# Kernel optimization log

Measured on AMD Instinct MI355X. Metric: run time of the kernel, lower is better.

## Reference

```python
import jax, jax.numpy as jnp
import numpy as np

B, T, D, H, KH, HD, F, L, V = 2, 2048, 1024, 16, 4, 64, 4096, 4, 32000
G = H // KH  # num_key_value_groups
EPS = 1e-6
SCALE = HD ** -0.5


def setup_inputs() -> dict:
    key = jax.random.key(0)
    ks = jax.random.split(key, 8)
    std = 0.02
    return {
        "input_ids": jax.random.randint(ks[0], (B, T), 0, V, dtype=jnp.int32),
        "embed_w": jax.random.normal(ks[1], (V, D), jnp.float32) * std,
        "pos_w": jax.random.normal(ks[2], (T, D), jnp.float32) * std,
        "ln1_w": jnp.ones((L, D), jnp.float32),
        "ln2_w": jnp.ones((L, D), jnp.float32),
        "wq": jax.random.normal(ks[3], (L, D, H * HD), jnp.float32) * std,
        "wkv": jax.random.normal(ks[4], (L, D, 2 * KH * HD), jnp.float32) * std,
        "wo": jax.random.normal(ks[5], (L, H * HD, D), jnp.float32) * std,
        "w1": jax.random.normal(ks[6], (L, D, F), jnp.float32) * std,
        "w2": jax.random.normal(ks[7], (L, F, D), jnp.float32) * std,
        "norm_w": jnp.ones((D,), jnp.float32),
    }


def _rmsnorm(x, w):
    return x * jax.lax.rsqrt(jnp.mean(x * x, axis=-1, keepdims=True) + EPS) * w


def reference(input_ids, embed_w, pos_w, ln1_w, ln2_w, wq, wkv, wo, w1, w2, norm_w):
    causal = jnp.tril(jnp.ones((T, T), dtype=bool))  # True = keep
    x = embed_w[input_ids] + pos_w[:T]  # [B,T,D]
    for l in range(L):
        h = _rmsnorm(x, ln1_w[l])
        q = (h @ wq[l]).reshape(B, T, H, HD)
        kv = h @ wkv[l]
        k, v = jnp.split(kv, 2, axis=-1)
        k = jnp.repeat(k.reshape(B, T, KH, HD), G, axis=2)  # GQA repeat_interleave
        v = jnp.repeat(v.reshape(B, T, KH, HD), G, axis=2)
        scores = jnp.einsum("bqhd,bkhd->bhqk", q, k) * SCALE
        scores = jnp.where(causal, scores, -jnp.inf)
        p = jax.nn.softmax(scores, axis=-1)
        o = jnp.einsum("bhqk,bkhd->bqhd", p, v).reshape(B, T, H * HD)
        x = x + o @ wo[l]
        h = _rmsnorm(x, ln2_w[l])
        x = x + jax.nn.gelu(h @ w1[l], approximate=False) @ w2[l]
    x = _rmsnorm(x, norm_w)
    logits = x @ embed_w.T  # tied lm_head
    return logits
```

## Files before the change

kernel.cpp:

```cpp
#include <hip/hip_runtime.h>
#include <hip/hip_bf16.h>

#define DI __device__ __forceinline__

typedef unsigned short u16;
typedef unsigned int u32;
typedef __attribute__((ext_vector_type(8))) short bf16x8;
typedef __attribute__((ext_vector_type(4))) short bf16x4;
typedef __attribute__((ext_vector_type(4))) float f32x4;

#define B_   2
#define T_   2048
#define D_   1024
#define H_   16
#define KH_  4
#define HD_  64
#define F_   4096
#define L_   4
#define V_   32000
#define M_   (B_ * T_)
#define QKVN (H_*HD_ + 2*KH_*HD_)

DI u16 f2bf(float f) {
  __hip_bfloat16 h = __float2bfloat16(f);
  return *reinterpret_cast<u16*>(&h);
}

DI float bf2f(u16 b) {
  __hip_bfloat16 h = *reinterpret_cast<__hip_bfloat16*>(&b);
  return __bfloat162float(h);
}

DI void gl_lds16(const void* g, void* l) {
  __builtin_amdgcn_global_load_lds(
      (const __attribute__((address_space(1))) u32*)g,
      (__attribute__((address_space(3))) u32*)l, 16, 0, 0);
}

#define BARRIER() do { asm volatile("" ::: "memory"); __builtin_amdgcn_s_barrier(); asm volatile("" ::: "memory"); } while (0)
#define LGK0()    asm volatile("s_waitcnt lgkmcnt(0)" ::: "memory")
#define VMC(n)    asm volatile("s_waitcnt vmcnt(" #n ")" ::: "memory")
#define PRIO(p)   __builtin_amdgcn_s_setprio(p)

__global__ __launch_bounds__(256) void embed_kernel(const int* __restrict__ ids,
                                                    const float* __restrict__ ew,
                                                    const float* __restrict__ pw,
                                                    float* __restrict__ x) {
  const int row = blockIdx.x;
  const int t = row & (T_ - 1);
  const int id = ids[row];
  float4 e = reinterpret_cast<const float4*>(ew + (size_t)id * D_)[threadIdx.x];
  float4 p = reinterpret_cast<const float4*>(pw + (size_t)t * D_)[threadIdx.x];
  e.x += p.x; e.y += p.y; e.z += p.z; e.w += p.w;
  reinterpret_cast<float4*>(x + (size_t)row * D_)[threadIdx.x] = e;
}

__global__ __launch_bounds__(256) void conv_kernel(const float* __restrict__ W,
                                                   u16* __restrict__ Wb) {
  const size_t i = (size_t)blockIdx.x * 256 + threadIdx.x;
  float4 v = reinterpret_cast<const float4*>(W)[i];
  ushort4 ov;
  ov.x = f2bf(v.x); ov.y = f2bf(v.y); ov.z = f2bf(v.z); ov.w = f2bf(v.w);
  reinterpret_cast<ushort4*>(Wb)[i] = ov;
}

__global__ __launch_bounds__(256) void convt_fused(const float* __restrict__ wq,
                                                   const float* __restrict__ wkv,
                                                   const float* __restrict__ wo,
                                                   const float* __restrict__ w1,
                                                   const float* __restrict__ w2,
                                                   u16* __restrict__ wtq,
                                                   u16* __restrict__ wto,
                                                   u16* __restrict__ wt1,
                                                   u16* __restrict__ wt2) {
  const int t = blockIdx.x;
  const float* W; u16* Wt; int K, N, local;
  if (t < 1024)      { W = wq;  Wt = wtq;               K = 1024; N = 1024; local = t; }
  else if (t < 1536) { W = wkv; Wt = wtq + 1024*1024;   K = 1024; N = 512;  local = t - 1024; }
  else if (t < 2560) { W = wo;  Wt = wto;               K = 1024; N = 1024; local = t - 1536; }
  else if (t < 6656) { W = w1;  Wt = wt1;               K = 1024; N = 4096; local = t - 2560; }
  else               { W = w2;  Wt = wt2;               K = 4096; N = 1024; local = t - 6656; }
  const int nk = K >> 5;
  const int k0 = (local % nk) * 32, n0 = (local / nk) * 32;
  __shared__ float tb[32][33];
  const int tx = threadIdx.x & 31, ty = threadIdx.x >> 5;
  #pragma unroll
  for (int i = 0; i < 4; i++)
    tb[ty + i*8][tx] = W[(size_t)(k0 + ty + i*8) * N + n0 + tx];
  __syncthreads();
  #pragma unroll
  for (int i = 0; i < 4; i++)
    Wt[(size_t)(n0 + ty + i*8) * K + k0 + tx] = f2bf(tb[tx][ty + i*8]);
}

__global__ __launch_bounds__(256) void rmsnorm_kernel(const float* __restrict__ x,
                                                      const float* __restrict__ w,
                                                      u16* __restrict__ out) {
  const int row = blockIdx.x;
  const int tid = threadIdx.x;
  float4 v = reinterpret_cast<const float4*>(x + (size_t)row * D_)[tid];
  float ss = v.x*v.x + v.y*v.y + v.z*v.z + v.w*v.w;
  #pragma unroll
  for (int off = 32; off > 0; off >>= 1) ss += __shfl_down(ss, off, 64);
  __shared__ float red[4];
  if ((tid & 63) == 0) red[tid >> 6] = ss;
  __syncthreads();
  const float tot = red[0] + red[1] + red[2] + red[3];
  const float rstd = rsqrtf(tot * (1.0f / D_) + 1e-6f);
  float4 wv = reinterpret_cast<const float4*>(w)[tid];
  ushort4 ov;
  ov.x = f2bf(v.x * rstd * wv.x);
  ov.y = f2bf(v.y * rstd * wv.y);
  ov.z = f2bf(v.z * rstd * wv.z);
  ov.w = f2bf(v.w * rstd * wv.w);
  reinterpret_cast<ushort4*>(out + (size_t)row * D_)[tid] = ov;
}

template <int EPI>
__global__ __launch_bounds__(256) void gemm_bt(const u16* __restrict__ A,
                                               const u16* __restrict__ Bt,
                                               const float* __restrict__ res,
                                               u16* __restrict__ Cb,
                                               float* __restrict__ Cf,
                                               int M, int N, int K) {
  __shared__ u16 As[128 * 64];
  __shared__ u16 Bs[128 * 64];
  const int tid = threadIdx.x;
  const int n0 = blockIdx.x * 128;
  const int m0 = blockIdx.y * 128;
  const int lane = tid & 63, wave = tid >> 6;
  const int wm = wave >> 1, wn = wave & 1;
  const int l15 = lane & 15, l4 = lane >> 4;
  const int srow = tid >> 3, scol = (tid & 7) * 8;
  const u16* ag = A + (size_t)(m0 + srow) * K + scol;
  const u16* bg = Bt + (size_t)(n0 + srow) * K + scol;
  u16* asd = &As[srow * 64 + scol];
  u16* bsd = &Bs[srow * 64 + scol];
  f32x4 acc[4][4] = {};
  const int nk = K >> 6;
  for (int kt = 0; kt < nk; kt++) {
    const int k0 = kt * 64;
    __syncthreads();
    #pragma unroll
    for (int i = 0; i < 4; i++) gl_lds16(ag + (size_t)i*32*K + k0, asd + i*32*64);
    #pragma unroll
    for (int i = 0; i < 4; i++) gl_lds16(bg + (size_t)i*32*K + k0, bsd + i*32*64);
    __syncthreads();
    #pragma unroll
    for (int s = 0; s < 2; s++) {
      bf16x8 af[4], bfv[4];
      #pragma unroll
      for (int i = 0; i < 4; i++)
        af[i] = *reinterpret_cast<const bf16x8*>(&As[(wm*64 + i*16 + l15)*64 + s*32 + l4*8]);
      #pragma unroll
      for (int j = 0; j < 4; j++)
        bfv[j] = *reinterpret_cast<const bf16x8*>(&Bs[(wn*64 + j*16 + l15)*64 + s*32 + l4*8]);
      #pragma unroll
      for (int i = 0; i < 4; i++)
        #pragma unroll
        for (int j = 0; j < 4; j++)
          acc[i][j] = __builtin_amdgcn_mfma_f32_16x16x32_bf16(bfv[j], af[i], acc[i][j], 0, 0, 0);
    }
  }
  #pragma unroll
  for (int i = 0; i < 4; i++) {
    const int row = m0 + wm*64 + i*16 + l15;
    #pragma unroll
    for (int j = 0; j < 4; j++) {
      const int colb = n0 + wn*64 + j*16 + l4*4;
      const size_t idx = (size_t)row * N + colb;
      const f32x4 v = acc[i][j];
      if (EPI == 0) {
        ushort4 ov;
        ov.x = f2bf(v[0]); ov.y = f2bf(v[1]); ov.z = f2bf(v[2]); ov.w = f2bf(v[3]);
        *reinterpret_cast<ushort4*>(&Cb[idx]) = ov;
      } else {
        const float4 rv = *reinterpret_cast<const float4*>(&res[idx]);
        float4 ov;
        ov.x = v[0] + rv.x; ov.y = v[1] + rv.y; ov.z = v[2] + rv.z; ov.w = v[3] + rv.w;
        *reinterpret_cast<float4*>(&Cf[idx]) = ov;
      }
    }
  }
}

template <int EPI>
__global__ __launch_bounds__(512, 2) void gemm256(const u16* __restrict__ A,
                                                  const u16* __restrict__ Bt,
                                                  u16* __restrict__ Cb,
                                                  float* __restrict__ Cf,
                                                  int M, int N, int K) {
  __shared__ char lds[131072];
  char* const AsB = lds;
  char* const BsB = lds + 65536;
  const int tid = threadIdx.x;
  const int lane = tid & 63, wave = tid >> 6;
  const int wm = wave >> 2, wn = wave & 3;
  const int l15 = lane & 15, l4 = lane >> 4;

  const int nm = M >> 8;
  const int nwg = nm * (N >> 8);
  const int cpx = nwg >> 3;
  const int bid = blockIdx.x;
  const int wg = (bid & 7) * cpx + (bid >> 3);
  const int m0 = (wg % nm) << 8;
  const int n0 = (wg / nm) << 8;

  const u16* const Atile = A + (size_t)m0 * K;
  const u16* const Btile = Bt + (size_t)n0 * K;

  int soff[2][2], pd[2][2];
  #pragma unroll
  for (int h = 0; h < 2; ++h)
    #pragma unroll
    for (int jj = 0; jj < 2; ++jj) {
      const int row = h*128 + jj*64 + (tid >> 3);
      const int sl  = (tid & 7) ^ (row & 7);
      soff[h][jj] = row * K + sl * 8;
      pd[h][jj]   = h*16384 + jj*8192 + tid*16;
    }
  const int swz = (l15 & 7) << 4;
  const int rb0 = l15*128 + ((l4*16)      ^ swz);
  const int rb1 = l15*128 + ((64 + l4*16) ^ swz);

  #define STA(S,H,T) do { const u16* g_ = Atile + (T)*64; char* d_ = AsB + (S)*32768; \
      gl_lds16(g_ + soff[H][0], d_ + pd[H][0]); gl_lds16(g_ + soff[H][1], d_ + pd[H][1]); } while (0)
  #define STB(S,H,T) do { const u16* g_ = Btile + (T)*64; char* d_ = BsB + (S)*32768; \
      gl_lds16(g_ + soff[H][0], d_ + pd[H][0]); gl_lds16(g_ + soff[H][1], d_ + pd[H][1]); } while (0)
  #define RDA(S,GI,RB) (*reinterpret_cast<const bf16x8*>(AsB + (S)*32768 + (GI)*2048 + (RB)))
  #define RDB(S,GJ,RB) (*reinterpret_cast<const bf16x8*>(BsB + (S)*32768 + (GJ)*2048 + (RB)))

  f32x4 acc[8][4] = {};
  bf16x8 Ar[4][2], Br[4][2];

  #define RDA03(S) { _Pragma("unroll") for (int i=0;i<4;++i){ Ar[i][0]=RDA(S,i*2+wm,rb0); Ar[i][1]=RDA(S,i*2+wm,rb1);} }
  #define RDA47(S) { _Pragma("unroll") for (int i=0;i<4;++i){ Ar[i][0]=RDA(S,(i+4)*2+wm,rb0); Ar[i][1]=RDA(S,(i+4)*2+wm,rb1);} }
  #define RDB01(S) { _Pragma("unroll") for (int j=0;j<2;++j){ Br[j][0]=RDB(S,j*4+wn,rb0); Br[j][1]=RDB(S,j*4+wn,rb1);} }
  #define RDB23(S) { _Pragma("unroll") for (int j=2;j<4;++j){ Br[j][0]=RDB(S,j*4+wn,rb0); Br[j][1]=RDB(S,j*4+wn,rb1);} }
  #define MFQ(IO,JL) { _Pragma("unroll") for (int i=0;i<4;++i) _Pragma("unroll") for (int jj=0;jj<2;++jj) { \
      acc[(IO)+i][(JL)+jj] = __builtin_amdgcn_mfma_f32_16x16x32_bf16(Br[(JL)+jj][0], Ar[i][0], acc[(IO)+i][(JL)+jj],0,0,0); \
      acc[(IO)+i][(JL)+jj] = __builtin_amdgcn_mfma_f32_16x16x32_bf16(Br[(JL)+jj][1], Ar[i][1], acc[(IO)+i][(JL)+jj],0,0,0); } }

  STA(0,0,0); STA(0,1,0); STB(0,0,0); STB(0,1,0);
  VMC(4);
  STA(1,0,1); STB(1,0,1); STB(1,1,1);
  VMC(6);
  BARRIER();

  const int niter = K >> 7;
  for (int it = 0; it < niter; ++it) {
    const int t0 = it*2, t1 = t0 + 1;
    const bool pf = (it + 1 < niter);
    RDA03(0); RDB01(0); STA(1,1,t1);
    BARRIER(); LGK0(); PRIO(1); MFQ(0,0); PRIO(0); BARRIER();
    RDB23(0); if (pf) STA(0,0,t0+2);
    BARRIER(); LGK0(); PRIO(1); MFQ(0,2); PRIO(0); BARRIER();
    RDA47(0); if (pf) STB(0,0,t0+2);
    BARRIER(); LGK0(); PRIO(1); MFQ(4,0); PRIO(0); BARRIER();
    if (pf) { STB(0,1,t0+2); VMC(6); } else { VMC(0); }
    BARRIER(); PRIO(1); MFQ(4,2); PRIO(0); BARRIER();
    RDA03(1); RDB01(1); if (pf) STA(0,1,t0+2);
    BARRIER(); LGK0(); PRIO(1); MFQ(0,0); PRIO(0); BARRIER();
    RDB23(1); if (pf) STA(1,0,t1+2);
    BARRIER(); LGK0(); PRIO(1); MFQ(0,2); PRIO(0); BARRIER();
    RDA47(1); if (pf) STB(1,0,t1+2);
    BARRIER(); LGK0(); PRIO(1); MFQ(4,0); PRIO(0); BARRIER();
    if (pf) { STB(1,1,t1+2); VMC(6); }
    BARRIER(); PRIO(1); MFQ(4,2); PRIO(0); BARRIER();
  }

  #pragma unroll
  for (int i = 0; i < 8; ++i) {
    const int row = m0 + (i*2 + wm)*16 + l15;
    #pragma unroll
    for (int j = 0; j < 4; ++j) {
      const int colb = n0 + (j*4 + wn)*16 + l4*4;
      const f32x4 v = acc[i][j];
      if (EPI == 0) {
        *reinterpret_cast<f32x4*>(&Cf[(size_t)row * N + colb]) = v;
      } else {
        ushort4 ov;
        #pragma unroll
        for (int rr = 0; rr < 4; ++rr) {
          const float g = 0.5f * v[rr] * (1.0f + erff(v[rr] * 0.70710678118f));
          ((u16*)&ov)[rr] = f2bf(g);
        }
        *reinterpret_cast<ushort4*>(&Cb[(size_t)row * N + colb]) = ov;
      }
    }
  }
  #undef STA
  #undef STB
  #undef RDA
  #undef RDB
  #undef RDA03
  #undef RDA47
  #undef RDB01
  #undef RDB23
  #undef MFQ
}

__global__ __launch_bounds__(512) void attn_kernel(const u16* __restrict__ qkv,
                                                   u16* __restrict__ o) {
  const int qtA = blockIdx.x;
  const int qtB = 15 - qtA;
  const int h  = blockIdx.y;
  const int b  = blockIdx.z;
  const int kh = h / (H_ / KH_);
  __shared__ u16 Ks[2][64 * 64];
  __shared__ u16 Vt[64 * 66];
  __shared__ u16 Pl[16][16 * 68];
  const int tid = threadIdx.x, lane = tid & 63, wave = tid >> 6;
  const int l15 = lane & 15, l4 = lane >> 4;
  const size_t Mrow = (size_t)b * T_;

  bf16x8 qfA[2], qfB[2];
  {
    const u16* qpA = qkv + (Mrow + qtA*128 + wave*16 + l15) * QKVN + h*HD_ + l4*8;
    const u16* qpB = qkv + (Mrow + qtB*128 + wave*16 + l15) * QKVN + h*HD_ + l4*8;
    qfA[0] = *reinterpret_cast<const bf16x8*>(qpA);
    qfA[1] = *reinterpret_cast<const bf16x8*>(qpA + 32);
    qfB[0] = *reinterpret_cast<const bf16x8*>(qpB);
    qfB[1] = *reinterpret_cast<const bf16x8*>(qpB + 32);
    #pragma unroll
    for (int s = 0; s < 2; s++)
      #pragma unroll
      for (int j = 0; j < 8; j++) {
        qfA[s][j] = (short)f2bf(bf2f((u16)qfA[s][j]) * 0.18033688f);
        qfB[s][j] = (short)f2bf(bf2f((u16)qfB[s][j]) * 0.18033688f);
      }
  }
  float mA = -1e30f, lA = 0.0f, mB = -1e30f, lB = 0.0f;
  f32x4 oaccA[4] = {}, oaccB[4] = {};

  const int srow = tid >> 3, scol = (tid & 7) * 8;
  const int vp = (tid >> 4) * 2;
  const int vd = (tid & 15) * 4;
  const u16* const kbase = qkv + Mrow * QKVN + D_ + kh*HD_;
  const u16* const vbase = kbase + KH_*HD_;

  {
    gl_lds16(kbase + (size_t)srow * QKVN + scol, &Ks[0][srow*64 + scol]);
    const u16* vg = vbase + (size_t)vp * QKVN + vd;
    bf16x4 v0 = *reinterpret_cast<const bf16x4*>(vg);
    bf16x4 v1 = *reinterpret_cast<const bf16x4*>(vg + QKVN);
    #pragma unroll
    for (int j = 0; j < 4; j++) {
      const u32 pk = (u32)(u16)v0[j] | ((u32)(u16)v1[j] << 16);
      *reinterpret_cast<u32*>(&Vt[(vd + j)*66 + vp]) = pk;
    }
  }
  __syncthreads();

  const int nktA = 2*qtA + 2;
  const int nktB = 2*qtB + 2;
  for (int kt = 0; kt < nktB; kt++) {
    const int cur = kt & 1;
    const bool pf = kt + 1 < nktB;
    bf16x4 v0n, v1n;
    if (pf) {
      gl_lds16(kbase + (size_t)((kt+1)*64 + srow) * QKVN + scol,
               &Ks[1-cur][srow*64 + scol]);
      const u16* vg = vbase + (size_t)((kt+1)*64 + vp) * QKVN + vd;
      v0n = *reinterpret_cast<const bf16x4*>(vg);
      v1n = *reinterpret_cast<const bf16x4*>(vg + QKVN);
    }

    {
      f32x4 sa[4] = {};
      #pragma unroll
      for (int s = 0; s < 2; s++)
        #pragma unroll
        for (int n = 0; n < 4; n++) {
          bf16x8 kf = *reinterpret_cast<const bf16x8*>(&Ks[cur][(n*16 + l15)*64 + s*32 + l4*8]);
          sa[n] = __builtin_amdgcn_mfma_f32_16x16x32_bf16(kf, qfB[s], sa[n], 0, 0, 0);
        }
      if (kt >= 2*qtB) {
        const int qloc = wave*16 + l15;
        const int kb = kt*64 - qtB*128 + l4*4;
        #pragma unroll
        for (int n = 0; n < 4; n++)
          #pragma unroll
          for (int r = 0; r < 4; r++)
            if (kb + n*16 + r > qloc) sa[n][r] = -1e30f;
      }
      float mx;
      {
        f32x4 m4;
        #pragma unroll
        for (int r = 0; r < 4; r++)
          m4[r] = fmaxf(fmaxf(sa[0][r], sa[1][r]), fmaxf(sa[2][r], sa[3][r]));
        mx = fmaxf(fmaxf(m4[0], m4[1]), fmaxf(m4[2], m4[3]));
        mx = fmaxf(mx, __shfl_xor(mx, 16, 64));
        mx = fmaxf(mx, __shfl_xor(mx, 32, 64));
      }
      if (__any((int)(mx - mB > 8.0f))) {
        const float nm = fmaxf(mB, mx);
        const float alpha = exp2f(mB - nm);
        mB = nm; lB *= alpha;
        #pragma unroll
        for (int r = 0; r < 4; r++) {
          const float a_r = __shfl(alpha, l4*4 + r, 64);
          #pragma unroll
          for (int n = 0; n < 4; n++) oaccB[n][r] *= a_r;
        }
      }
      float rs = 0.0f;
      u16* pw = &Pl[8 + wave][0];
      #pragma unroll
      for (int n = 0; n < 4; n++) {
        ushort4 pv;
        #pragma unroll
        for (int r = 0; r < 4; r++) {
          const float p = exp2f(sa[n][r] - mB);
          rs += p;
          ((u16*)&pv)[r] = f2bf(p);
        }
        *reinterpret_cast<ushort4*>(&pw[l15*68 + n*16 + l4*4]) = pv;
      }
      rs += __shfl_xor(rs, 16, 64);
      rs += __shfl_xor(rs, 32, 64);
      lB += rs;
      asm volatile("s_waitcnt lgkmcnt(0)" ::: "memory");
      #pragma unroll
      for (int s = 0; s < 2; s++) {
        bf16x8 pa = *reinterpret_cast<const bf16x8*>(&pw[l15*68 + s*32 + l4*8]);
        #pragma unroll
        for (int n = 0; n < 4; n++) {
          bf16x8 vb = *reinterpret_cast<const bf16x8*>(&Vt[(n*16 + l15)*66 + s*32 + l4*8]);
          oaccB[n] = __builtin_amdgcn_mfma_f32_16x16x32_bf16(pa, vb, oaccB[n], 0, 0, 0);
        }
      }
    }

    if (kt < nktA) {
      f32x4 sa[4] = {};
      #pragma unroll
      for (int s = 0; s < 2; s++)
        #pragma unroll
        for (int n = 0; n < 4; n++) {
          bf16x8 kf = *reinterpret_cast<const bf16x8*>(&Ks[cur][(n*16 + l15)*64 + s*32 + l4*8]);
          sa[n] = __builtin_amdgcn_mfma_f32_16x16x32_bf16(kf, qfA[s], sa[n], 0, 0, 0);
        }
      if (kt >= 2*qtA) {
        const int qloc = wave*16 + l15;
        const int kb = kt*64 - qtA*128 + l4*4;
        #pragma unroll
        for (int n = 0; n < 4; n++)
          #pragma unroll
          for (int r = 0; r < 4; r++)
            if (kb + n*16 + r > qloc) sa[n][r] = -1e30f;
      }
      float mx;
      {
        f32x4 m4;
        #pragma unroll
        for (int r = 0; r < 4; r++)
          m4[r] = fmaxf(fmaxf(sa[0][r], sa[1][r]), fmaxf(sa[2][r], sa[3][r]));
        mx = fmaxf(fmaxf(m4[0], m4[1]), fmaxf(m4[2], m4[3]));
        mx = fmaxf(mx, __shfl_xor(mx, 16, 64));
        mx = fmaxf(mx, __shfl_xor(mx, 32, 64));
      }
      if (__any((int)(mx - mA > 8.0f))) {
        const float nm = fmaxf(mA, mx);
        const float alpha = exp2f(mA - nm);
        mA = nm; lA *= alpha;
        #pragma unroll
        for (int r = 0; r < 4; r++) {
          const float a_r = __shfl(alpha, l4*4 + r, 64);
          #pragma unroll
          for (int n = 0; n < 4; n++) oaccA[n][r] *= a_r;
        }
      }
      float rs = 0.0f;
      u16* pw = &Pl[wave][0];
      #pragma unroll
      for (int n = 0; n < 4; n++) {
        ushort4 pv;
        #pragma unroll
        for (int r = 0; r < 4; r++) {
          const float p = exp2f(sa[n][r] - mA);
          rs += p;
          ((u16*)&pv)[r] = f2bf(p);
        }
        *reinterpret_cast<ushort4*>(&pw[l15*68 + n*16 + l4*4]) = pv;
      }
      rs += __shfl_xor(rs, 16, 64);
      rs += __shfl_xor(rs, 32, 64);
      lA += rs;
      asm volatile("s_waitcnt lgkmcnt(0)" ::: "memory");
      #pragma unroll
      for (int s = 0; s < 2; s++) {
        bf16x8 pa = *reinterpret_cast<const bf16x8*>(&pw[l15*68 + s*32 + l4*8]);
        #pragma unroll
        for (int n = 0; n < 4; n++) {
          bf16x8 vb = *reinterpret_cast<const bf16x8*>(&Vt[(n*16 + l15)*66 + s*32 + l4*8]);
          oaccA[n] = __builtin_amdgcn_mfma_f32_16x16x32_bf16(pa, vb, oaccA[n], 0, 0, 0);
        }
      }
    }

    __syncthreads();
    if (pf) {
      #pragma unroll
      for (int j = 0; j < 4; j++) {
        const u32 pk = (u32)(u16)v0n[j] | ((u32)(u16)v1n[j] << 16);
        *reinterpret_cast<u32*>(&Vt[(vd + j)*66 + vp]) = pk;
      }
      __syncthreads();
    }
  }
  {
    float lr[4];
    #pragma unroll
    for (int r = 0; r < 4; r++) lr[r] = __shfl(lA, l4*4 + r, 64);
    #pragma unroll
    for (int n = 0; n < 4; n++)
      #pragma unroll
      for (int r = 0; r < 4; r++) {
        const float ov = oaccA[n][r] / lr[r];
        const size_t row = Mrow + qtA*128 + wave*16 + l4*4 + r;
        o[row * (size_t)(H_*HD_) + h*HD_ + n*16 + l15] = f2bf(ov);
      }
    #pragma unroll
    for (int r = 0; r < 4; r++) lr[r] = __shfl(lB, l4*4 + r, 64);
    #pragma unroll
    for (int n = 0; n < 4; n++)
      #pragma unroll
      for (int r = 0; r < 4; r++) {
        const float ov = oaccB[n][r] / lr[r];
        const size_t row = Mrow + qtB*128 + wave*16 + l4*4 + r;
        o[row * (size_t)(H_*HD_) + h*HD_ + n*16 + l15] = f2bf(ov);
      }
  }
}

#define OFF_X     0ull
#define OFF_H     16777216ull
#define OFF_QKV   25165824ull
#define OFF_O     37748736ull
#define OFF_U     46137344ull
#define OFF_WTQ   79691776ull
#define OFF_WTO   82837504ull
#define OFF_WT1   84934656ull
#define OFF_WT2   93323264ull
#define OFF_EBF   101711872ull

extern "C" void kernel_launch(void* const* d_in, const int* in_sizes, int n_in,
                              void* d_out, int out_size, void* d_ws, size_t ws_size,
                              hipStream_t stream) {
  const int*   ids = (const int*)  d_in[0];
  const float* ew  = (const float*)d_in[1];
  const float* pw  = (const float*)d_in[2];
  const float* ln1 = (const float*)d_in[3];
  const float* ln2 = (const float*)d_in[4];
  const float* wq  = (const float*)d_in[5];
  const float* wkv = (const float*)d_in[6];
  const float* wo  = (const float*)d_in[7];
  const float* w1  = (const float*)d_in[8];
  const float* w2  = (const float*)d_in[9];
  const float* nw  = (const float*)d_in[10];
  float* out = (float*)d_out;

  char* ws = (char*)d_ws;
  float* x   = (float*)(ws + OFF_X);
  u16*   h   = (u16*)  (ws + OFF_H);
  u16*   qkv = (u16*)  (ws + OFF_QKV);
  u16*   o   = (u16*)  (ws + OFF_O);
  u16*   u   = (u16*)  (ws + OFF_U);
  u16*   wtq = (u16*)  (ws + OFF_WTQ);
  u16*   wto = (u16*)  (ws + OFF_WTO);
  u16*   wt1 = (u16*)  (ws + OFF_WT1);
  u16*   wt2 = (u16*)  (ws + OFF_WT2);
  u16*   ebf = (u16*)  (ws + OFF_EBF);

  embed_kernel<<<M_, 256, 0, stream>>>(ids, ew, pw, x);
  conv_kernel<<<(V_*D_/4)/256, 256, 0, stream>>>(ew, ebf);

  for (int l = 0; l < L_; l++) {
    convt_fused<<<10752, 256, 0, stream>>>(
        wq  + (size_t)l*D_*(H_*HD_),
        wkv + (size_t)l*D_*(2*KH_*HD_),
        wo  + (size_t)l*(H_*HD_)*D_,
        w1  + (size_t)l*D_*F_,
        w2  + (size_t)l*F_*D_,
        wtq, wto, wt1, wt2);

    rmsnorm_kernel<<<M_, 256, 0, stream>>>(x, ln1 + (size_t)l*D_, h);
    gemm_bt<0><<<dim3(QKVN/128, M_/128), 256, 0, stream>>>(h, wtq, nullptr, qkv, nullptr, M_, QKVN, D_);
    attn_kernel<<<dim3(T_/256, H_, B_), 512, 0, stream>>>(qkv, o);
    gemm_bt<1><<<dim3(D_/128, M_/128), 256, 0, stream>>>(o, wto, x, nullptr, x, M_, D_, H_*HD_);
    rmsnorm_kernel<<<M_, 256, 0, stream>>>(x, ln2 + (size_t)l*D_, h);
    gemm256<1><<<dim3((F_/256)*(M_/256)), 512, 0, stream>>>(h, wt1, u, nullptr, M_, F_, D_);
    gemm_bt<1><<<dim3(D_/128, M_/128), 256, 0, stream>>>(u, wt2, x, nullptr, x, M_, D_, F_);
  }

  rmsnorm_kernel<<<M_, 256, 0, stream>>>(x, nw, h);
  gemm256<0><<<dim3((V_/256)*(M_/256)), 512, 0, stream>>>(h, ebf, nullptr, out, M_, V_, D_);
}
```

Before: 1.598 ms.

## Remap GEMM blocks across XCDs and double-buffer V tile in attention

The gemm_bt kernel now uses a 1D grid and remaps block IDs so that consecutive tiles land on the same XCD (bid&7 chunking), which is meant to improve L2 locality on the multi-die MI355X. In attention, the transposed V tile becomes double-buffered: the next tile's V is written to the alternate buffer during the current iteration. This removes the second __syncthreads per iteration, at the cost of extra LDS. The remap assumes the tile count divides evenly by 8.

Result: faster. 1.475 ms (-7.7%).

```diff
diff --git a/kernel.cpp b/kernel.cpp
--- a/kernel.cpp
+++ b/kernel.cpp
@@ -126,8 +126,13 @@
   __shared__ u16 As[128 * 64];
   __shared__ u16 Bs[128 * 64];
   const int tid = threadIdx.x;
-  const int n0 = blockIdx.x * 128;
-  const int m0 = blockIdx.y * 128;
+  const int nx = N >> 7;
+  const int nwg = nx * (M >> 7);
+  const int cpx = nwg >> 3;
+  const int bid = blockIdx.x;
+  const int wg = (bid & 7) * cpx + (bid >> 3);
+  const int n0 = (wg % nx) << 7;
+  const int m0 = (wg / nx) << 7;
   const int lane = tid & 63, wave = tid >> 6;
   const int wm = wave >> 1, wn = wave & 1;
   const int l15 = lane & 15, l4 = lane >> 4;
@@ -308,7 +313,7 @@
   const int b  = blockIdx.z;
   const int kh = h / (H_ / KH_);
   __shared__ u16 Ks[2][64 * 64];
-  __shared__ u16 Vt[64 * 66];
+  __shared__ u16 Vt[2][64 * 66];
   __shared__ u16 Pl[16][16 * 68];
   const int tid = threadIdx.x, lane = tid & 63, wave = tid >> 6;
   const int l15 = lane & 15, l4 = lane >> 4;
@@ -347,7 +352,7 @@
     #pragma unroll
     for (int j = 0; j < 4; j++) {
       const u32 pk = (u32)(u16)v0[j] | ((u32)(u16)v1[j] << 16);
-      *reinterpret_cast<u32*>(&Vt[(vd + j)*66 + vp]) = pk;
+      *reinterpret_cast<u32*>(&Vt[0][(vd + j)*66 + vp]) = pk;
     }
   }
   __syncthreads();
@@ -366,30 +371,30 @@
       v1n = *reinterpret_cast<const bf16x4*>(vg + QKVN);
     }
 
+    f32x4 saB[4] = {};
+    #pragma unroll
+    for (int s = 0; s < 2; s++)
+      #pragma unroll
+      for (int n = 0; n < 4; n++) {
+        bf16x8 kf = *reinterpret_cast<const bf16x8*>(&Ks[cur][(n*16 + l15)*64 + s*32 + l4*8]);
+        saB[n] = __builtin_amdgcn_mfma_f32_16x16x32_bf16(kf, qfB[s], saB[n], 0, 0, 0);
+      }
+    if (kt >= 2*qtB) {
+      const int qloc = wave*16 + l15;
+      const int kb = kt*64 - qtB*128 + l4*4;
+      #pragma unroll
+      for (int n = 0; n < 4; n++)
+        #pragma unroll
+        for (int r = 0; r < 4; r++)
+          if (kb + n*16 + r > qloc) saB[n][r] = -1e30f;
+    }
     {
-      f32x4 sa[4] = {};
-      #pragma unroll
-      for (int s = 0; s < 2; s++)
-        #pragma unroll
-        for (int n = 0; n < 4; n++) {
-          bf16x8 kf = *reinterpret_cast<const bf16x8*>(&Ks[cur][(n*16 + l15)*64 + s*32 + l4*8]);
-          sa[n] = __builtin_amdgcn_mfma_f32_16x16x32_bf16(kf, qfB[s], sa[n], 0, 0, 0);
-        }
-      if (kt >= 2*qtB) {
-        const int qloc = wave*16 + l15;
-        const int kb = kt*64 - qtB*128 + l4*4;
-        #pragma unroll
-        for (int n = 0; n < 4; n++)
-          #pragma unroll
-          for (int r = 0; r < 4; r++)
-            if (kb + n*16 + r > qloc) sa[n][r] = -1e30f;
-      }
       float mx;
       {
         f32x4 m4;
         #pragma unroll
         for (int r = 0; r < 4; r++)
-          m4[r] = fmaxf(fmaxf(sa[0][r], sa[1][r]), fmaxf(sa[2][r], sa[3][r]));
+          m4[r] = fmaxf(fmaxf(saB[0][r], saB[1][r]), fmaxf(saB[2][r], saB[3][r]));
         mx = fmaxf(fmaxf(m4[0], m4[1]), fmaxf(m4[2], m4[3]));
         mx = fmaxf(mx, __shfl_xor(mx, 16, 64));
         mx = fmaxf(mx, __shfl_xor(mx, 32, 64));
@@ -412,7 +417,7 @@
         ushort4 pv;
         #pragma unroll
         for (int r = 0; r < 4; r++) {
-          const float p = exp2f(sa[n][r] - mB);
+          const float p = exp2f(saB[n][r] - mB);
           rs += p;
           ((u16*)&pv)[r] = f2bf(p);
         }
@@ -421,15 +426,24 @@
       rs += __shfl_xor(rs, 16, 64);
       rs += __shfl_xor(rs, 32, 64);
       lB += rs;
-      asm volatile("s_waitcnt lgkmcnt(0)" ::: "memory");
-      #pragma unroll
-      for (int s = 0; s < 2; s++) {
-        bf16x8 pa = *reinterpret_cast<const bf16x8*>(&pw[l15*68 + s*32 + l4*8]);
-        #pragma unroll
-        for (int n = 0; n < 4; n++) {
-          bf16x8 vb = *reinterpret_cast<const bf16x8*>(&Vt[(n*16 + l15)*66 + s*32 + l4*8]);
-          oaccB[n] = __builtin_amdgcn_mfma_f32_16x16x32_bf16(pa, vb, oaccB[n], 0, 0, 0);
-        }
+    }
+
+    if (pf) {
+      #pragma unroll
+      for (int j = 0; j < 4; j++) {
+        const u32 pk = (u32)(u16)v0n[j] | ((u32)(u16)v1n[j] << 16);
+        *reinterpret_cast<u32*>(&Vt[1-cur][(vd + j)*66 + vp]) = pk;
+      }
+    }
+
+    asm volatile("s_waitcnt lgkmcnt(0)" ::: "memory");
+    #pragma unroll
+    for (int s = 0; s < 2; s++) {
+      bf16x8 pa = *reinterpret_cast<const bf16x8*>(&Pl[8 + wave][l15*68 + s*32 + l4*8]);
+      #pragma unroll
+      for (int n = 0; n < 4; n++) {
+        bf16x8 vb = *reinterpret_cast<const bf16x8*>(&Vt[cur][(n*16 + l15)*66 + s*32 + l4*8]);
+        oaccB[n] = __builtin_amdgcn_mfma_f32_16x16x32_bf16(pa, vb, oaccB[n], 0, 0, 0);
       }
     }
 
@@ -494,21 +508,13 @@
         bf16x8 pa = *reinterpret_cast<const bf16x8*>(&pw[l15*68 + s*32 + l4*8]);
         #pragma unroll
         for (int n = 0; n < 4; n++) {
-          bf16x8 vb = *reinterpret_cast<const bf16x8*>(&Vt[(n*16 + l15)*66 + s*32 + l4*8]);
+          bf16x8 vb = *reinterpret_cast<const bf16x8*>(&Vt[cur][(n*16 + l15)*66 + s*32 + l4*8]);
           oaccA[n] = __builtin_amdgcn_mfma_f32_16x16x32_bf16(pa, vb, oaccA[n], 0, 0, 0);
         }
       }
     }
 
     __syncthreads();
-    if (pf) {
-      #pragma unroll
-      for (int j = 0; j < 4; j++) {
-        const u32 pk = (u32)(u16)v0n[j] | ((u32)(u16)v1n[j] << 16);
-        *reinterpret_cast<u32*>(&Vt[(vd + j)*66 + vp]) = pk;
-      }
-      __syncthreads();
-    }
   }
   {
     float lr[4];
@@ -587,12 +593,12 @@
         wtq, wto, wt1, wt2);
 
     rmsnorm_kernel<<<M_, 256, 0, stream>>>(x, ln1 + (size_t)l*D_, h);
-    gemm_bt<0><<<dim3(QKVN/128, M_/128), 256, 0, stream>>>(h, wtq, nullptr, qkv, nullptr, M_, QKVN, D_);
+    gemm_bt<0><<<(QKVN/128)*(M_/128), 256, 0, stream>>>(h, wtq, nullptr, qkv, nullptr, M_, QKVN, D_);
     attn_kernel<<<dim3(T_/256, H_, B_), 512, 0, stream>>>(qkv, o);
-    gemm_bt<1><<<dim3(D_/128, M_/128), 256, 0, stream>>>(o, wto, x, nullptr, x, M_, D_, H_*HD_);
+    gemm_bt<1><<<(D_/128)*(M_/128), 256, 0, stream>>>(o, wto, x, nullptr, x, M_, D_, H_*HD_);
     rmsnorm_kernel<<<M_, 256, 0, stream>>>(x, ln2 + (size_t)l*D_, h);
     gemm256<1><<<dim3((F_/256)*(M_/256)), 512, 0, stream>>>(h, wt1, u, nullptr, M_, F_, D_);
-    gemm_bt<1><<<dim3(D_/128, M_/128), 256, 0, stream>>>(u, wt2, x, nullptr, x, M_, D_, F_);
+    gemm_bt<1><<<(D_/128)*(M_/128), 256, 0, stream>>>(u, wt2, x, nullptr, x, M_, D_, F_);
   }
 
   rmsnorm_kernel<<<M_, 256, 0, stream>>>(x, nw, h);
```
